# Kernel optimization log

Hardware: AMD Instinct MI355X
Metric: run time of the kernel (lower is better)

Reference implementation:

```python
import math
import jax, jax.numpy as jnp
import numpy as np

# static config (mirrors init_kwargs / input_specs)
B, HRV, WRV, CRV = 2, 32, 1024, 64
CB, HB, WB = 256, 200, 200
D, COUT, HEADS, POINTS = 128, 128, 8, 6
DH = D // HEADS
RMAX = 55.0
XMIN, XMAX, YMIN, YMAX = -50.0, 50.0, -50.0, 50.0


def group_norm(x, gamma, beta, groups, eps=1e-5):
    b, h, w, c = x.shape
    xg = x.reshape(b, h, w, groups, c // groups)
    mean = xg.mean(axis=(1, 2, 4), keepdims=True)
    var = xg.var(axis=(1, 2, 4), keepdims=True)
    xg = (xg - mean) * jax.lax.rsqrt(var + eps)
    return xg.reshape(b, h, w, c) * gamma + beta


def fwd(x_rv, bev, pq_w, pq_b, pv_w, pv_b, po_w, po_b, qs_w1, qs_b1, qs_w2, qs_b2,
        rh_w1, rh_b1, rh_g1, rh_be1, rh_w2, rh_g2, rh_be2, rh_w3, rh_b3,
        so_w, so_b, aw_w, aw_b, vp_w, vp_b, op_w, op_b):
    b = x_rv.shape[0]
    nq = HRV * WRV
    az = jnp.linspace(-math.pi, math.pi, WRV + 1)[:-1]  # [Wrv]
    az = jnp.broadcast_to(az[None, None, :], (b, HRV, WRV))
    coord = jnp.stack([jnp.sin(az), jnp.cos(az), jnp.zeros_like(az)], axis=-1)  # [b,H,W,3]
    Q0 = x_rv @ pq_w + pq_b                                  # 1x1 conv as matmul (NHWC)
    Vmap = bev.transpose(0, 2, 3, 1) @ pv_w + pv_b           # [b,HB,WB,D]
    # range head: 1x1 conv -> GN(8) -> GELU -> 3x3 circular conv -> GN(8) -> GELU -> 1x1 conv
    h = jnp.concatenate([x_rv, coord], axis=-1) @ rh_w1 + rh_b1
    h = jax.nn.gelu(group_norm(h, rh_g1, rh_be1, 8), approximate=False)
    hp = jnp.pad(h, ((0, 0), (1, 1), (1, 1), (0, 0)), mode='wrap')  # circular padding
    h = jax.lax.conv_general_dilated(hp, rh_w2, (1, 1), 'VALID',
                                     dimension_numbers=('NHWC', 'HWIO', 'NHWC'))
    h = jax.nn.gelu(group_norm(h, rh_g2, rh_be2, 8), approximate=False)
    rh = h @ rh_w3 + rh_b3                                   # [b,H,W,2]
    mu = jnp.clip(rh[..., 0], 0.0, RMAX)                     # [b,H,W]
    log_sigma = jnp.clip(rh[..., 1:2], -5.0, 3.0)            # [b,H,W,1]
    sigma = jnp.exp(log_sigma)
    x_mu = mu * jnp.cos(az)
    y_mu = mu * jnp.sin(az)
    rx = jnp.clip((x_mu - XMIN) / (XMAX - XMIN), 0.0, 1.0)
    ry = jnp.clip((y_mu - YMIN) / (YMAX - YMIN), 0.0, 1.0)
    ref = jnp.stack([rx, ry], axis=-1).reshape(b, nq, 2)
    sig_feat = jnp.concatenate([log_sigma, 1.0 / (sigma + 1e-6)], axis=-1)
    q = jnp.concatenate([Q0, sig_feat], axis=-1) @ qs_w1 + qs_b1
    q = jax.nn.gelu(q, approximate=False) @ qs_w2 + qs_b2
    query = q.reshape(b, nq, D)
    # ---- MSDA (num_levels = 1) ----
    value = Vmap.reshape(b, HB * WB, D) @ vp_w + vp_b
    vflat = value.reshape(b, HB * WB, HEADS, DH).transpose(0, 2, 1, 3)  # [b,heads,NV,dh]
    offs = (query @ so_w + so_b).reshape(b, nq, HEADS, POINTS, 2)
    attw = jax.nn.softmax((query @ aw_w + aw_b).reshape(b, nq, HEADS, POINTS), axis=-1)
    norm = jnp.array([WB, HB], dtype=query.dtype)            # offset_normalizer = [W, H]
    loc = ref[:, :, None, None, :] + offs / norm             # [b,nq,heads,P,2] in [0,1]
    loc = loc.transpose(0, 2, 1, 3, 4)                       # [b,heads,nq,P,2]
    attw = attw.transpose(0, 2, 1, 3)                        # [b,heads,nq,P]
    # grid_sample bilinear, zero padding, align_corners=False: pix = loc*size - 0.5
    px = loc[..., 0] * WB - 0.5
    py = loc[..., 1] * HB - 0.5
    x0 = jnp.floor(px).astype(jnp.int32)
    y0 = jnp.floor(py).astype(jnp.int32)
    wx = px - x0
    wy = py - y0

    def gather(xi, yi):
        valid = (xi >= 0) & (xi < WB) & (yi >= 0) & (yi < HB)
        idx = jnp.clip(yi, 0, HB - 1) * WB + jnp.clip(xi, 0, WB - 1)
        g = jnp.take_along_axis(vflat, idx.reshape(b, HEADS, nq * POINTS, 1), axis=2)
        return g.reshape(b, HEADS, nq, POINTS, DH) * valid[..., None]

    sampled = (gather(x0, y0) * ((1 - wx) * (1 - wy))[..., None]
               + gather(x0 + 1, y0) * (wx * (1 - wy))[..., None]
               + gather(x0, y0 + 1) * ((1 - wx) * wy)[..., None]
               + gather(x0 + 1, y0 + 1) * (wx * wy)[..., None])    # [b,heads,nq,P,dh]
    out = (sampled * attw[..., None]).sum(axis=3)                  # [b,heads,nq,dh]
    out = out.transpose(0, 2, 1, 3).reshape(b, nq, D) @ op_w + op_b
    y = out.reshape(b, HRV, WRV, D) @ po_w + po_b                  # proj_o (1x1 conv)
    return y                                                       # [b,Hrv,Wrv,C_out]


def setup_inputs() -> dict:
    key = jax.random.key(0)
    ks = jax.random.split(key, 20)
    def rn(i, shape, s=0.02):
        return s * jax.random.normal(ks[i], shape, jnp.float32)
    z = lambda n: jnp.zeros((n,), jnp.float32)
    o = lambda n: jnp.ones((n,), jnp.float32)
    return dict(
        x_rv=rn(0, (B, HRV, WRV, CRV), 1.0),
        bev=rn(1, (B, CB, HB, WB), 1.0),
        pq_w=rn(2, (CRV, D)), pq_b=z(D),
        pv_w=rn(3, (CB, D)), pv_b=z(D),
        po_w=rn(4, (D, COUT)), po_b=z(COUT),
        qs_w1=rn(5, (D + 2, D)), qs_b1=z(D),
        qs_w2=rn(6, (D, D)), qs_b2=z(D),
        rh_w1=rn(7, (CRV + 3, 128)), rh_b1=z(128),
        rh_g1=o(128), rh_be1=z(128),
        rh_w2=rn(8, (3, 3, 128, 64)),
        rh_g2=o(64), rh_be2=z(64),
        rh_w3=rn(9, (64, 2)), rh_b3=z(2),
        so_w=rn(10, (D, HEADS * POINTS * 2)), so_b=rn(11, (HEADS * POINTS * 2,), 0.5),
        aw_w=rn(12, (D, HEADS * POINTS)), aw_b=z(HEADS * POINTS),
        vp_w=rn(13, (D, D)), vp_b=z(D),
        op_w=rn(14, (D, D)), op_b=z(D),
    )


def reference(x_rv, bev, pq_w, pq_b, pv_w, pv_b, po_w, po_b, qs_w1, qs_b1, qs_w2, qs_b2,
              rh_w1, rh_b1, rh_g1, rh_be1, rh_w2, rh_g2, rh_be2, rh_w3, rh_b3,
              so_w, so_b, aw_w, aw_b, vp_w, vp_b, op_w, op_b):
    return fwd(x_rv, bev, pq_w, pq_b, pv_w, pv_b, po_w, po_b, qs_w1, qs_b1, qs_w2, qs_b2,
               rh_w1, rh_b1, rh_g1, rh_be1, rh_w2, rh_g2, rh_be2, rh_w3, rh_b3,
               so_w, so_b, aw_w, aw_b, vp_w, vp_b, op_w, op_b)
```

## Files before the change

### kernel.cpp

```cpp
#include <hip/hip_runtime.h>
#include <math.h>

#define PI_F 3.14159265358979323846f


typedef __attribute__((ext_vector_type(8))) short bf16x8;
typedef __attribute__((ext_vector_type(4))) float f32x4;

__device__ __forceinline__ float gelu_f(float x) {
    return 0.5f * x * (1.0f + erff(x * 0.70710678118654752440f));
}

__device__ __forceinline__ unsigned short f2bf(float x) {
    unsigned int u = __float_as_uint(x);
    u += 0x7fffu + ((u >> 16) & 1u);
    return (unsigned short)(u >> 16);
}

__device__ __forceinline__ float bf2f(unsigned short h) {
    return __uint_as_float((unsigned int)h << 16);
}

__global__ void prep_weights(const float* __restrict__ pv_w, const float* __restrict__ pv_b,
                             const float* __restrict__ vp_w, const float* __restrict__ vp_b,
                             const float* __restrict__ op_w, const float* __restrict__ op_b,
                             const float* __restrict__ po_w, const float* __restrict__ po_b,
                             const float* __restrict__ pq_w, const float* __restrict__ pq_b,
                             const float* __restrict__ qs_w1, const float* __restrict__ qs_b1,
                             const float* __restrict__ qs_w2, const float* __restrict__ qs_b2,
                             const float* __restrict__ so_w, const float* __restrict__ so_b,
                             const float* __restrict__ aw_w, const float* __restrict__ aw_b,
                             const float* __restrict__ rh_w2,
                             unsigned short* __restrict__ wvh, unsigned short* __restrict__ wvl,
                             float* __restrict__ pvvp_b,
                             float* __restrict__ oppo_w, float* __restrict__ oppo_b,
                             float* __restrict__ pqqs_w, float* __restrict__ pqqs_b,
                             float* __restrict__ qsso_w, float* __restrict__ qsso_b,
                             float* __restrict__ qsaw_w, float* __restrict__ qsaw_b,
                             unsigned short* __restrict__ wtb,
                             float2* __restrict__ azsc) {
    int r = blockIdx.x;
    int d = threadIdx.x;
    if (r < 256) {
        float s = 0.f;
        for (int k = 0; k < 128; ++k) s += pv_w[r * 128 + k] * vp_w[k * 128 + d];
        unsigned short h = f2bf(s);
        wvh[d * 256 + r] = h;
        wvl[d * 256 + r] = f2bf(s - bf2f(h));
    } else if (r == 256) {
        float s = vp_b[d];
        for (int k = 0; k < 128; ++k) s += pv_b[k] * vp_w[k * 128 + d];
        pvvp_b[d] = s;
    } else if (r < 385) {
        int rr = r - 257;
        float s = 0.f;
        for (int k = 0; k < 128; ++k) s += op_w[rr * 128 + k] * po_w[k * 128 + d];
        oppo_w[rr * 128 + d] = s;
    } else if (r == 385) {
        float s = po_b[d];
        for (int k = 0; k < 128; ++k) s += op_b[k] * po_w[k * 128 + d];
        oppo_b[d] = s;
    } else if (r < 450) {
        int rr = r - 386;
        float s = 0.f;
        for (int k = 0; k < 128; ++k) s += pq_w[rr * 128 + k] * qs_w1[k * 128 + d];
        pqqs_w[rr * 128 + d] = s;
    } else if (r == 450) {
        float s = qs_b1[d];
        for (int k = 0; k < 128; ++k) s += pq_b[k] * qs_w1[k * 128 + d];
        pqqs_b[d] = s;
    } else if (r < 459) {
        int w = (r - 451) * 128 + d;
        float az = -PI_F + (float)w * (6.283185307179586f / 1024.0f);
        azsc[w] = make_float2(sinf(az), cosf(az));
    } else if (r < 587) {
        int rr = r - 459;
        if (d < 96) {
            float s = 0.f;
            for (int k = 0; k < 128; ++k) s += qs_w2[rr * 128 + k] * so_w[k * 96 + d];
            qsso_w[rr * 96 + d] = s;
        }
    } else if (r == 587) {
        if (d < 96) {
            float s = so_b[d];
            for (int k = 0; k < 128; ++k) s += qs_b2[k] * so_w[k * 96 + d];
            qsso_b[d] = s;
        }
    } else if (r < 716) {
        int rr = r - 588;
        if (d < 48) {
            float s = 0.f;
            for (int k = 0; k < 128; ++k) s += qs_w2[rr * 128 + k] * aw_w[k * 48 + d];
            qsaw_w[rr * 48 + d] = s;
        }
    } else if (r == 716) {
        if (d < 48) {
            float s = aw_b[d];
            for (int k = 0; k < 128; ++k) s += qs_b2[k] * aw_w[k * 48 + d];
            qsaw_b[d] = s;
        }
    } else {
        int idx = (r - 717) * 128 + d;
        int ci = idx & 31;
        int o = (idx >> 5) & 63;
        int cc4i = (idx >> 11) & 3;
        int tap = idx >> 13;
        float w = rh_w2[((size_t)tap * 128 + cc4i * 32 + ci) * 64 + o];
        wtb[idx] = f2bf(w);
    }
}

template <int NT, bool STATS>
__global__ __launch_bounds__(2 * NT) void gemm_v3(
    const float* __restrict__ A, int lda,
    const float* __restrict__ W,
    const float* __restrict__ bias,
    float* __restrict__ C, int K,
    const float2* __restrict__ azsc,
    const float* __restrict__ extra2,
    const float* __restrict__ extra_w,
    int emode, int do_gelu, float* __restrict__ stats1) {
    constexpr int NTH = 2 * NT;
    constexpr int NTO = NT / 8;
    __shared__ float As[32][140];
    __shared__ float Ws[32][NT];
    __shared__ float sred[8][2];
    const int tid = threadIdx.x;
    const int tn = tid % NTO;
    const int tm = tid / NTO;
    const int m0 = blockIdx.x * 128;
    if (STATS && tid < 16) sred[tid >> 1][tid & 1] = 0.f;
    float acc[8][8];
#pragma unroll
    for (int i = 0; i < 8; ++i)
#pragma unroll
        for (int j = 0; j < 8; ++j) acc[i][j] = 0.f;

    for (int k0 = 0; k0 < K; k0 += 32) {
        __syncthreads();
        for (int f = tid; f < 1024; f += NTH) {
            int r = f >> 3, c4 = f & 7;
            float4 v = *(const float4*)(A + (size_t)(m0 + r) * lda + k0 + c4 * 4);
            As[c4 * 4 + 0][r] = v.x;
            As[c4 * 4 + 1][r] = v.y;
            As[c4 * 4 + 2][r] = v.z;
            As[c4 * 4 + 3][r] = v.w;
        }
        for (int f = tid; f < 8 * NT; f += NTH) {
            int kk = f / (NT / 4), n4 = f % (NT / 4);
            *(float4*)&Ws[kk][n4 * 4] = *(const float4*)(W + (size_t)(k0 + kk) * NT + n4 * 4);
        }
        __syncthreads();
#pragma unroll 2
        for (int k = 0; k < 32; ++k) {
            const float4 a0 = *(const float4*)&As[k][tm * 8];
            const float4 a1 = *(const float4*)&As[k][tm * 8 + 4];
            const float4 w0 = *(const float4*)&Ws[k][tn * 8];
            const float4 w1 = *(const float4*)&Ws[k][tn * 8 + 4];
            const float av[8] = {a0.x, a0.y, a0.z, a0.w, a1.x, a1.y, a1.z, a1.w};
            const float wv[8] = {w0.x, w0.y, w0.z, w0.w, w1.x, w1.y, w1.z, w1.w};
#pragma unroll
            for (int i = 0; i < 8; ++i)
#pragma unroll
                for (int j = 0; j < 8; ++j) acc[i][j] += av[i] * wv[j];
        }
    }
    float bv[8], e0w[8], e1w[8];
#pragma unroll
    for (int j = 0; j < 8; ++j) bv[j] = bias[tn * 8 + j];
    if (emode) {
#pragma unroll
        for (int j = 0; j < 8; ++j) {
            e0w[j] = extra_w[tn * 8 + j];
            e1w[j] = extra_w[NT + tn * 8 + j];
        }
    }
    float ts = 0.f, ts2 = 0.f;
#pragma unroll
    for (int i = 0; i < 8; ++i) {
        int m = m0 + tm * 8 + i;
        float e0 = 0.f, e1 = 0.f;
        if (emode == 1) {
            float2 sc = azsc[m & 1023];
            e0 = sc.x; e1 = sc.y;
        } else if (emode == 2) {
            e0 = extra2[2 * (size_t)m];
            e1 = extra2[2 * (size_t)m + 1];
        }
        float o[8];
#pragma unroll
        for (int j = 0; j < 8; ++j) {
            float v = acc[i][j] + bv[j];
            if (emode) v += e0 * e0w[j] + e1 * e1w[j];
            if (do_gelu) v = gelu_f(v);
            if (STATS) { ts += v; ts2 += v * v; }
            o[j] = v;
        }
        *(float4*)(C + (size_t)m * NT + tn * 8) = make_float4(o[0], o[1], o[2], o[3]);
        *(float4*)(C + (size_t)m * NT + tn * 8 + 4) = make_float4(o[4], o[5], o[6], o[7]);
    }
    if (STATS) {
        atomicAdd(&sred[tn >> 1][0], ts);
        atomicAdd(&sred[tn >> 1][1], ts2);
        __syncthreads();
        if (tid < 8) {
            int b = m0 >> 15;
            atomicAdd(&stats1[(b * 8 + tid) * 2 + 0], sred[tid][0]);
            atomicAdd(&stats1[(b * 8 + tid) * 2 + 1], sred[tid][1]);
        }
    }
}

template <int MT, int NT, int NTH>
__global__ __launch_bounds__(NTH) void gemm_rn(
    const float* __restrict__ A, int lda,
    const float* __restrict__ W, int ldw,
    const float* __restrict__ bias,
    float* __restrict__ C, int ldc, int K) {
    static_assert(NTH == (MT / 8) * (NT / 4), "thread count mismatch");
    __shared__ float As[32][MT + 12];
    __shared__ float Ws[32][NT];
    constexpr int NTN = NT / 4;
    const int tid = threadIdx.x;
    const int tn = tid % NTN;
    const int tm = tid / NTN;
    const int m0 = blockIdx.x * MT;
    float acc[8][4];
#pragma unroll
    for (int i = 0; i < 8; ++i)
#pragma unroll
        for (int j = 0; j < 4; ++j) acc[i][j] = 0.f;

    for (int k0 = 0; k0 < K; k0 += 32) {
        __syncthreads();
        for (int f = tid; f < MT * 8; f += NTH) {
            int r = f >> 3, c4 = f & 7;
            float4 v = *(const float4*)(A + (size_t)(m0 + r) * lda + k0 + c4 * 4);
            As[c4 * 4 + 0][r] = v.x;
            As[c4 * 4 + 1][r] = v.y;
            As[c4 * 4 + 2][r] = v.z;
            As[c4 * 4 + 3][r] = v.w;
        }
        for (int f = tid; f < 8 * NT; f += NTH) {
            int kk = f / NTN, n4 = f % NTN;
            *(float4*)&Ws[kk][n4 * 4] = *(const float4*)(W + (size_t)(k0 + kk) * ldw + n4 * 4);
        }
        __syncthreads();
#pragma unroll 4
        for (int k = 0; k < 32; ++k) {
            const float4 a0 = *(const float4*)&As[k][tm * 8];
            const float4 a1 = *(const float4*)&As[k][tm * 8 + 4];
            const float4 wv = *(const float4*)&Ws[k][tn * 4];
            acc[0][0] += a0.x * wv.x; acc[0][1] += a0.x * wv.y; acc[0][2] += a0.x * wv.z; acc[0][3] += a0.x * wv.w;
            acc[1][0] += a0.y * wv.x; acc[1][1] += a0.y * wv.y; acc[1][2] += a0.y * wv.z; acc[1][3] += a0.y * wv.w;
            acc[2][0] += a0.z * wv.x; acc[2][1] += a0.z * wv.y; acc[2][2] += a0.z * wv.z; acc[2][3] += a0.z * wv.w;
            acc[3][0] += a0.w * wv.x; acc[3][1] += a0.w * wv.y; acc[3][2] += a0.w * wv.z; acc[3][3] += a0.w * wv.w;
            acc[4][0] += a1.x * wv.x; acc[4][1] += a1.x * wv.y; acc[4][2] += a1.x * wv.z; acc[4][3] += a1.x * wv.w;
            acc[5][0] += a1.y * wv.x; acc[5][1] += a1.y * wv.y; acc[5][2] += a1.y * wv.z; acc[5][3] += a1.y * wv.w;
            acc[6][0] += a1.z * wv.x; acc[6][1] += a1.z * wv.y; acc[6][2] += a1.z * wv.z; acc[6][3] += a1.z * wv.w;
            acc[7][0] += a1.w * wv.x; acc[7][1] += a1.w * wv.y; acc[7][2] += a1.w * wv.z; acc[7][3] += a1.w * wv.w;
        }
    }
#pragma unroll
    for (int i = 0; i < 8; ++i) {
        int m = m0 + tm * 8 + i;
        float4 o;
        o.x = acc[i][0] + bias[tn * 4 + 0];
        o.y = acc[i][1] + bias[tn * 4 + 1];
        o.z = acc[i][2] + bias[tn * 4 + 2];
        o.w = acc[i][3] + bias[tn * 4 + 3];
        *(float4*)(C + (size_t)m * ldc + tn * 4) = o;
    }
}

__global__ __launch_bounds__(256) void value_gemm_mfma(
    const float* __restrict__ bev,
    const unsigned short* __restrict__ Wh, const unsigned short* __restrict__ Wl,
    const float* __restrict__ bf, float* __restrict__ V) {
    __shared__ __align__(16) short Ah_s[128 * 40];
    __shared__ __align__(16) short Al_s[128 * 40];
    __shared__ __align__(16) short Bh_s[128 * 40];
    __shared__ __align__(16) short Bl_s[128 * 40];
    const int tid = threadIdx.x;
    const int wid = tid >> 6;
    const int lane = tid & 63;
    const int m = lane & 15;
    const int quad = lane >> 4;
    const int n0 = blockIdx.x * 128;
    const int b = blockIdx.y;
    const float* bevb = bev + (size_t)b * 256 * 40000;
    const int wr = (wid >> 1) * 64;
    const int wc = (wid & 1) * 64;
    f32x4 acc[4][4];
#pragma unroll
    for (int i = 0; i < 4; ++i)
#pragma unroll
        for (int j = 0; j < 4; ++j) acc[i][j] = (f32x4){0.f, 0.f, 0.f, 0.f};

    const int sn = tid & 127;
    const int kq0 = (tid >> 7) * 2;
    int ng = n0 + sn;
    if (ng > 39999) ng = 39999;
    const float* srcA = bevb + ng;

    float va[2][8];
#define LOADA(K0)                                                        \
    {                                                                    \
        _Pragma("unroll")                                                \
        for (int i_ = 0; i_ < 2; ++i_) {                                 \
            const float* s_ = srcA + (size_t)((K0) + (kq0 + i_) * 8) * 40000; \
            _Pragma("unroll")                                            \
            for (int j_ = 0; j_ < 8; ++j_) va[i_][j_] = s_[(size_t)j_ * 40000]; \
        }                                                                \
    }

    LOADA(0);
    for (int k0 = 0; k0 < 256; k0 += 32) {
        __syncthreads();
#pragma unroll
        for (int i = 0; i < 2; ++i) {
            int k8 = kq0 + i;
            bf16x8 ph, pl;
#pragma unroll
            for (int j = 0; j < 8; ++j) {
                unsigned short h = f2bf(va[i][j]);
                ph[j] = (short)h;
                pl[j] = (short)f2bf(va[i][j] - bf2f(h));
            }
            *(bf16x8*)&Ah_s[sn * 40 + k8 * 8] = ph;
            *(bf16x8*)&Al_s[sn * 40 + k8 * 8] = pl;
        }
        if (k0 < 224) LOADA(k0 + 32);
        for (int f = tid; f < 512; f += 256) {
            int d = f >> 2, k8 = f & 3;
            uint4 vh = *(const uint4*)(Wh + (size_t)d * 256 + k0 + k8 * 8);
            uint4 vl = *(const uint4*)(Wl + (size_t)d * 256 + k0 + k8 * 8);
            *(uint4*)&Bh_s[d * 40 + k8 * 8] = vh;
            *(uint4*)&Bl_s[d * 40 + k8 * 8] = vl;
        }
        __syncthreads();
        bf16x8 ah[4], al[4], bh[4], bl[4];
#pragma unroll
        for (int r = 0; r < 4; ++r) {
            ah[r] = *(const bf16x8*)&Ah_s[(wr + r * 16 + m) * 40 + quad * 8];
            al[r] = *(const bf16x8*)&Al_s[(wr + r * 16 + m) * 40 + quad * 8];
            bh[r] = *(const bf16x8*)&Bh_s[(wc + r * 16 + m) * 40 + quad * 8];
            bl[r] = *(const bf16x8*)&Bl_s[(wc + r * 16 + m) * 40 + quad * 8];
        }
#pragma unroll
        for (int i = 0; i < 4; ++i)
#pragma unroll
            for (int j = 0; j < 4; ++j) {
                acc[i][j] = __builtin_amdgcn_mfma_f32_16x16x32_bf16(ah[i], bh[j], acc[i][j], 0, 0, 0);
                acc[i][j] = __builtin_amdgcn_mfma_f32_16x16x32_bf16(ah[i], bl[j], acc[i][j], 0, 0, 0);
                acc[i][j] = __builtin_amdgcn_mfma_f32_16x16x32_bf16(al[i], bh[j], acc[i][j], 0, 0, 0);
            }
    }
#undef LOADA
    float bv[4];
#pragma unroll
    for (int j = 0; j < 4; ++j) bv[j] = bf[wc + j * 16 + m];
#pragma unroll
    for (int i = 0; i < 4; ++i) {
        int nbase = n0 + wr + i * 16 + quad * 4;
#pragma unroll
        for (int r = 0; r < 4; ++r) {
            int n = nbase + r;
            if (n < 40000) {
                float* vp = V + ((size_t)b * 40000 + n) * 128 + wc + m;
#pragma unroll
                for (int j = 0; j < 4; ++j) vp[j * 16] = acc[i][j][r] + bv[j];
            }
        }
    }
}

__global__ __launch_bounds__(256) void gn1_bf16(
    const float* __restrict__ X, const float* __restrict__ stats,
    const float* __restrict__ g1, const float* __restrict__ be1,
    unsigned short* __restrict__ Ob) {
    size_t i4 = (size_t)blockIdx.x * 256 + threadIdx.x;
    size_t base = i4 * 4;
    int c = (int)(base & 127);
    int mrow = (int)(base >> 7);
    int b = mrow >> 15;
    int g = c >> 4;
    float mean = stats[(b * 8 + g) * 2 + 0] * (1.0f / 524288.0f);
    float var = stats[(b * 8 + g) * 2 + 1] * (1.0f / 524288.0f) - mean * mean;
    float rs = 1.0f / sqrtf(var + 1e-5f);
    float4 x = *(const float4*)(X + base);
    float4 gm = *(const float4*)(g1 + c);
    float4 bt = *(const float4*)(be1 + c);
    ushort4 o;
    o.x = f2bf(gelu_f((x.x - mean) * rs * gm.x + bt.x));
    o.y = f2bf(gelu_f((x.y - mean) * rs * gm.y + bt.y));
    o.z = f2bf(gelu_f((x.z - mean) * rs * gm.z + bt.z));
    o.w = f2bf(gelu_f((x.w - mean) * rs * gm.w + bt.w));
    *(ushort4*)(Ob + base) = o;
}

__global__ __launch_bounds__(256, 4) void conv3x3_mfma(
    const unsigned short* __restrict__ H1b,
    const unsigned short* __restrict__ Wtb,
    float* __restrict__ Y,
    float* __restrict__ stats2) {
    __shared__ short As_s[66 * 40];
    __shared__ short Ws_s[3 * 64 * 40];
    __shared__ float sred[8][2];
    const int tid = threadIdx.x;
    const int wid = tid >> 6;
    const int lane = tid & 63;
    const int m = lane & 15;
    const int quad = lane >> 4;
    const int x0 = blockIdx.x * 64;
    const int y = blockIdx.y;
    const int b = blockIdx.z;
    if (tid < 16) sred[tid >> 1][tid & 1] = 0.f;
    f32x4 acc[4];
#pragma unroll
    for (int oq = 0; oq < 4; ++oq) acc[oq] = (f32x4){0.f, 0.f, 0.f, 0.f};

    const unsigned short* Hb = H1b + (size_t)b * 32 * 1024 * 128;
    for (int ry = 0; ry < 3; ++ry) {
        const int gy = (y + ry + 31) & 31;
        const unsigned short* Hrow = Hb + (size_t)gy * 1024 * 128;
        for (int cc4 = 0; cc4 < 4; ++cc4) {
            __syncthreads();
            for (int f = tid; f < 264; f += 256) {
                int xx = f >> 2, cq = f & 3;
                int gx = (x0 + xx + 1023) & 1023;
                uint4 v = *(const uint4*)(Hrow + (size_t)gx * 128 + cc4 * 32 + cq * 8);
                *(uint4*)&As_s[xx * 40 + cq * 8] = v;
            }
            for (int f = tid; f < 768; f += 256) {
                int cq = f & 3, o = (f >> 2) & 63, dx = f >> 8;
                int tap = ry * 3 + dx;
                uint4 v = *(const uint4*)(Wtb + ((size_t)(tap * 4 + cc4) * 64 + o) * 32 + cq * 8);
                *(uint4*)&Ws_s[(dx * 64 + o) * 40 + cq * 8] = v;
            }
            __syncthreads();
            const int arow = wid * 16 + m;
#pragma unroll
            for (int dx = 0; dx < 3; ++dx) {
                bf16x8 a = *(const bf16x8*)&As_s[(arow + dx) * 40 + quad * 8];
#pragma unroll
                for (int oq = 0; oq < 4; ++oq) {
                    bf16x8 bfr = *(const bf16x8*)&Ws_s[(dx * 64 + oq * 16 + m) * 40 + quad * 8];
                    acc[oq] = __builtin_amdgcn_mfma_f32_16x16x32_bf16(a, bfr, acc[oq], 0, 0, 0);
                }
            }
        }
    }
    float sv[4], qv[4];
#pragma unroll
    for (int oq = 0; oq < 4; ++oq) {
        sv[oq] = acc[oq].x + acc[oq].y + acc[oq].z + acc[oq].w;
        qv[oq] = acc[oq].x * acc[oq].x + acc[oq].y * acc[oq].y +
                 acc[oq].z * acc[oq].z + acc[oq].w * acc[oq].w;
    }
    const int masks[5] = {1, 2, 4, 16, 32};
#pragma unroll
    for (int mi = 0; mi < 5; ++mi) {
#pragma unroll
        for (int oq = 0; oq < 4; ++oq) {
            sv[oq] += __shfl_xor(sv[oq], masks[mi]);
            qv[oq] += __shfl_xor(qv[oq], masks[mi]);
        }
    }
    if ((lane & 55) == 0) {
        int gb = (lane >> 3) & 1;
#pragma unroll
        for (int oq = 0; oq < 4; ++oq) {
            atomicAdd(&sred[oq * 2 + gb][0], sv[oq]);
            atomicAdd(&sred[oq * 2 + gb][1], qv[oq]);
        }
    }
    const int pxb = x0 + wid * 16 + quad * 4;
    float* Yb = Y + ((size_t)(b * 32 + y) * 1024 + pxb) * 64;
#pragma unroll
    for (int oq = 0; oq < 4; ++oq) {
        const float av[4] = {acc[oq].x, acc[oq].y, acc[oq].z, acc[oq].w};
#pragma unroll
        for (int r = 0; r < 4; ++r) Yb[(size_t)r * 64 + oq * 16 + m] = av[r];
    }
    __syncthreads();
    if (tid < 16)
        atomicAdd(&stats2[(b * 8 + (tid >> 1)) * 2 + (tid & 1)], sred[tid >> 1][tid & 1]);
}

__global__ __launch_bounds__(256) void rh3_kernel(
    const float* __restrict__ H2, const float* __restrict__ stats,
    const float* __restrict__ gamma, const float* __restrict__ beta, float inv_cnt,
    const float* __restrict__ w3, const float* __restrict__ b3,
    const float2* __restrict__ azsc,
    float2* __restrict__ refxy, float2* __restrict__ sigf) {
    const int tid = threadIdx.x;
    const int lane = tid & 15;
    const int m = blockIdx.x * 16 + (tid >> 4);
    const int b = m >> 15;
    const int c = lane * 4;
    const int g = c >> 3;
    float mean = stats[(b * 8 + g) * 2 + 0] * inv_cnt;
    float var = stats[(b * 8 + g) * 2 + 1] * inv_cnt - mean * mean;
    float rs = 1.0f / sqrtf(var + 1e-5f);
    float4 v = *(const float4*)(H2 + (size_t)m * 64 + c);
    float hv[4];
    hv[0] = gelu_f((v.x - mean) * rs * gamma[c + 0] + beta[c + 0]);
    hv[1] = gelu_f((v.y - mean) * rs * gamma[c + 1] + beta[c + 1]);
    hv[2] = gelu_f((v.z - mean) * rs * gamma[c + 2] + beta[c + 2]);
    hv[3] = gelu_f((v.w - mean) * rs * gamma[c + 3] + beta[c + 3]);
    float d0 = 0.f, d1 = 0.f;
#pragma unroll
    for (int k = 0; k < 4; ++k) {
        d0 += hv[k] * w3[(c + k) * 2 + 0];
        d1 += hv[k] * w3[(c + k) * 2 + 1];
    }
#pragma unroll
    for (int s = 1; s < 16; s <<= 1) {
        d0 += __shfl_xor(d0, s, 16);
        d1 += __shfl_xor(d1, s, 16);
    }
    if (lane == 0) {
        float mu = fminf(fmaxf(d0 + b3[0], 0.f), 55.f);
        float ls = fminf(fmaxf(d1 + b3[1], -5.f), 3.f);
        float sg = expf(ls);
        float2 sc = azsc[m & 1023];
        float rx = fminf(fmaxf(mu * sc.y * 0.01f + 0.5f, 0.f), 1.f);
        float ry = fminf(fmaxf(mu * sc.x * 0.01f + 0.5f, 0.f), 1.f);
        refxy[m] = make_float2(rx, ry);
        sigf[m] = make_float2(ls, 1.f / (sg + 1e-6f));
    }
}

__global__ __launch_bounds__(256) void msda_kernel(
    const float* __restrict__ V, const float2* __restrict__ refxy,
    const float* __restrict__ offs, const float* __restrict__ aw,
    float* __restrict__ out) {
    const int tid = threadIdx.x;
    const int l4 = tid & 3;
    const int grp = tid >> 2;
    const int m = blockIdx.x * 8 + (grp >> 3);
    const int head = grp & 7;
    const int b = m >> 15;
    float2 r = refxy[m];
    const float* lg = aw + (size_t)m * 48 + head * 6;
    float l[6];
#pragma unroll
    for (int p = 0; p < 6; ++p) l[p] = lg[p];
    float mx = l[0];
#pragma unroll
    for (int p = 1; p < 6; ++p) mx = fmaxf(mx, l[p]);
    float s = 0.f;
#pragma unroll
    for (int p = 0; p < 6; ++p) { l[p] = expf(l[p] - mx); s += l[p]; }
    float inv = 1.f / s;
#pragma unroll
    for (int p = 0; p < 6; ++p) l[p] *= inv;
    const float* of = offs + (size_t)m * 96 + head * 12;
    const float* Vb = V + (size_t)b * 40000 * 128 + head * 16 + l4 * 4;
    const float bx = r.x * 200.f - 0.5f;
    const float by = r.y * 200.f - 0.5f;
    f32x4 acc = (f32x4){0.f, 0.f, 0.f, 0.f};
#pragma unroll
    for (int p = 0; p < 6; ++p) {
        float px = bx + of[p * 2 + 0];
        float py = by + of[p * 2 + 1];
        float fx = floorf(px), fy = floorf(py);
        int x0 = (int)fx, y0 = (int)fy;
        float wx = px - fx, wy = py - fy;
        int xc0 = min(max(x0, 0), 199), xc1 = min(max(x0 + 1, 0), 199);
        int yc0 = min(max(y0, 0), 199), yc1 = min(max(y0 + 1, 0), 199);
        bool vx0 = ((unsigned)x0 < 200u), vx1 = ((unsigned)(x0 + 1) < 200u);
        bool vy0 = ((unsigned)y0 < 200u), vy1 = ((unsigned)(y0 + 1) < 200u);
        const f32x4 v00 = *(const f32x4*)(Vb + ((size_t)(yc0 * 200 + xc0)) * 128);
        const f32x4 v10 = *(const f32x4*)(Vb + ((size_t)(yc0 * 200 + xc1)) * 128);
        const f32x4 v01 = *(const f32x4*)(Vb + ((size_t)(yc1 * 200 + xc0)) * 128);
        const f32x4 v11 = *(const f32x4*)(Vb + ((size_t)(yc1 * 200 + xc1)) * 128);
        float w = l[p];
        float w00 = (vx0 && vy0) ? w * (1.f - wx) * (1.f - wy) : 0.f;
        float w10 = (vx1 && vy0) ? w * wx * (1.f - wy) : 0.f;
        float w01 = (vx0 && vy1) ? w * (1.f - wx) * wy : 0.f;
        float w11 = (vx1 && vy1) ? w * wx * wy : 0.f;
        acc += v00 * w00;
        acc += v10 * w10;
        acc += v01 * w01;
        acc += v11 * w11;
    }
    *(f32x4*)(out + (size_t)m * 128 + head * 16 + l4 * 4) = acc;
}

extern "C" void kernel_launch(void* const* d_in, const int* in_sizes, int n_in,
                              void* d_out, int out_size, void* d_ws, size_t ws_size,
                              hipStream_t stream) {
    const float* x_rv = (const float*)d_in[0];
    const float* bev = (const float*)d_in[1];
    const float* pq_w = (const float*)d_in[2];
    const float* pq_b = (const float*)d_in[3];
    const float* pv_w = (const float*)d_in[4];
    const float* pv_b = (const float*)d_in[5];
    const float* po_w = (const float*)d_in[6];
    const float* po_b = (const float*)d_in[7];
    const float* qs_w1 = (const float*)d_in[8];
    const float* qs_b1 = (const float*)d_in[9];
    const float* qs_w2 = (const float*)d_in[10];
    const float* qs_b2 = (const float*)d_in[11];
    const float* rh_w1 = (const float*)d_in[12];
    const float* rh_b1 = (const float*)d_in[13];
    const float* rh_g1 = (const float*)d_in[14];
    const float* rh_be1 = (const float*)d_in[15];
    const float* rh_w2 = (const float*)d_in[16];
    const float* rh_g2 = (const float*)d_in[17];
    const float* rh_be2 = (const float*)d_in[18];
    const float* rh_w3 = (const float*)d_in[19];
    const float* rh_b3 = (const float*)d_in[20];
    const float* so_w = (const float*)d_in[21];
    const float* so_b = (const float*)d_in[22];
    const float* aw_w = (const float*)d_in[23];
    const float* aw_b = (const float*)d_in[24];
    const float* vp_w = (const float*)d_in[25];
    const float* vp_b = (const float*)d_in[26];
    const float* op_w = (const float*)d_in[27];
    const float* op_b = (const float*)d_in[28];

    const int M = 65536;

    float* ws = (float*)d_ws;
    float* azsc = ws;    ws += 2048;
    unsigned short* wvh = (unsigned short*)ws; ws += 16384;
    unsigned short* wvl = (unsigned short*)ws; ws += 16384;
    float* pvvp_b = ws;  ws += 128;
    float* oppo_w = ws;  ws += 128 * 128;
    float* oppo_b = ws;  ws += 128;
    float* pqqs_w = ws;  ws += 64 * 128;
    float* pqqs_b = ws;  ws += 128;
    float* qsso_w = ws;  ws += 128 * 96;
    float* qsso_b = ws;  ws += 128;
    float* qsaw_w = ws;  ws += 128 * 48;
    float* qsaw_b = ws;  ws += 64;
    float* stats = ws;   ws += 64;
    unsigned short* wtb = (unsigned short*)ws;  ws += 36864;
    unsigned short* h1b = (unsigned short*)ws;  ws += (size_t)M * 64;
    float* Vv = ws;      ws += (size_t)80000 * 128;
    float* h1 = ws;      ws += (size_t)M * 128;
    float* h2 = ws;      ws += (size_t)M * 64;
    float* q1 = ws;      ws += (size_t)M * 128;
    float* refxy = ws;   ws += (size_t)M * 2;
    float* sigf = ws;    ws += (size_t)M * 2;
    size_t need_bytes = (size_t)(ws - (float*)d_ws) * sizeof(float);
    if (ws_size < need_bytes) return;
    float* offs = h1;
    float* attw = h2;
    float* mo = q1;

    float2* azsc2 = (float2*)azsc;
    float2* refxy2 = (float2*)refxy;
    float2* sigf2 = (float2*)sigf;

    prep_weights<<<1293, 128, 0, stream>>>(
        pv_w, pv_b, vp_w, vp_b, op_w, op_b, po_w, po_b, pq_w, pq_b,
        qs_w1, qs_b1, qs_w2, qs_b2, so_w, so_b, aw_w, aw_b, rh_w2,
        wvh, wvl, pvvp_b, oppo_w, oppo_b, pqqs_w, pqqs_b,
        qsso_w, qsso_b, qsaw_w, qsaw_b, wtb, azsc2);
    hipMemsetAsync(stats, 0, 64 * sizeof(float), stream);

    gemm_v3<128, true><<<M / 128, 256, 0, stream>>>(
        x_rv, 64, rh_w1, rh_b1, h1, 64, azsc2, nullptr, rh_w1 + 64 * 128, 1, 0, stats);

    value_gemm_mfma<<<dim3(313, 2), 256, 0, stream>>>(bev, wvh, wvl, pvvp_b, Vv);

    gn1_bf16<<<8192, 256, 0, stream>>>(h1, stats, rh_g1, rh_be1, h1b);

    conv3x3_mfma<<<dim3(16, 32, 2), 256, 0, stream>>>(h1b, wtb, h2, stats + 32);

    rh3_kernel<<<4096, 256, 0, stream>>>(h2, stats + 32, rh_g2, rh_be2, 1.0f / 262144.0f,
                                         rh_w3, rh_b3, azsc2, refxy2, sigf2);

    gemm_v3<128, false><<<M / 128, 256, 0, stream>>>(
        x_rv, 64, pqqs_w, pqqs_b, q1, 64, nullptr, sigf, qs_w1 + 128 * 128, 2, 1, nullptr);

    gemm_v3<96, false><<<M / 128, 192, 0, stream>>>(
        q1, 128, qsso_w, qsso_b, offs, 128, nullptr, nullptr, nullptr, 0, 0, nullptr);

    gemm_rn<128, 48, 192><<<M / 128, 192, 0, stream>>>(
        q1, 128, qsaw_w, 48, qsaw_b, attw, 48, 128);

    msda_kernel<<<M / 8, 256, 0, stream>>>(Vv, refxy2, offs, attw, mo);

    gemm_v3<128, false><<<M / 128, 256, 0, stream>>>(
        mo, 128, oppo_w, oppo_b, (float*)d_out, 128, nullptr, nullptr, nullptr, 0, 0, nullptr);
}
```

Measured before the change: 480.1 us.

## Restructure BEV value GEMM: 64-row tiles, register-resident weights, double-buffered LDS

Cuts the value-projection tile from 128 to 64 rows, which doubles the grid to 625x2 blocks. Each wave now loads its bf16 hi/lo weight fragments straight from global memory into registers instead of staging them in LDS. The A tile is double-buffered in LDS so each k-step needs one barrier instead of two. The hi/lo bf16 split is now done with bit masking and a packed convert instruction rather than per-element rounding, and the bounds check is dropped because 40000 divides evenly by 64. In exchange, weight reads hit global or cache more often and each wave reuses less data per k-step.

```diff
diff --git a/kernel.cpp b/kernel.cpp
--- a/kernel.cpp
+++ b/kernel.cpp
@@ -277,100 +277,115 @@
     const float* __restrict__ bev,
     const unsigned short* __restrict__ Wh, const unsigned short* __restrict__ Wl,
     const float* __restrict__ bf, float* __restrict__ V) {
-    __shared__ __align__(16) short Ah_s[128 * 40];
-    __shared__ __align__(16) short Al_s[128 * 40];
-    __shared__ __align__(16) short Bh_s[128 * 40];
-    __shared__ __align__(16) short Bl_s[128 * 40];
+    __shared__ __align__(16) short Ah0_s[64 * 40];
+    __shared__ __align__(16) short Al0_s[64 * 40];
+    __shared__ __align__(16) short Ah1_s[64 * 40];
+    __shared__ __align__(16) short Al1_s[64 * 40];
     const int tid = threadIdx.x;
     const int wid = tid >> 6;
     const int lane = tid & 63;
     const int m = lane & 15;
     const int quad = lane >> 4;
-    const int n0 = blockIdx.x * 128;
+    const int n0 = blockIdx.x * 64;
     const int b = blockIdx.y;
-    const float* bevb = bev + (size_t)b * 256 * 40000;
-    const int wr = (wid >> 1) * 64;
+    const int wr = (wid >> 1) * 32;
     const int wc = (wid & 1) * 64;
-    f32x4 acc[4][4];
-#pragma unroll
-    for (int i = 0; i < 4; ++i)
+    f32x4 acc[2][4];
+#pragma unroll
+    for (int i = 0; i < 2; ++i)
 #pragma unroll
         for (int j = 0; j < 4; ++j) acc[i][j] = (f32x4){0.f, 0.f, 0.f, 0.f};
 
-    const int sn = tid & 127;
-    const int kq0 = (tid >> 7) * 2;
-    int ng = n0 + sn;
-    if (ng > 39999) ng = 39999;
-    const float* srcA = bevb + ng;
-
-    float va[2][8];
-#define LOADA(K0)                                                        \
-    {                                                                    \
-        _Pragma("unroll")                                                \
-        for (int i_ = 0; i_ < 2; ++i_) {                                 \
-            const float* s_ = srcA + (size_t)((K0) + (kq0 + i_) * 8) * 40000; \
-            _Pragma("unroll")                                            \
-            for (int j_ = 0; j_ < 8; ++j_) va[i_][j_] = s_[(size_t)j_ * 40000]; \
-        }                                                                \
-    }
-
-    LOADA(0);
-    for (int k0 = 0; k0 < 256; k0 += 32) {
-        __syncthreads();
+    const int sn = tid & 63;
+    const int kq = tid >> 6;
+    const float* srcA = bev + (size_t)b * 256 * 40000 + n0 + sn;
+    const unsigned short* pBh[4];
+    const unsigned short* pBl[4];
+#pragma unroll
+    for (int j = 0; j < 4; ++j) {
+        size_t off = (size_t)(wc + j * 16 + m) * 256 + quad * 8;
+        pBh[j] = Wh + off;
+        pBl[j] = Wl + off;
+    }
+
+    float va[8];
+    bf16x8 vbh[4], vbl[4];
+#pragma unroll
+    for (int j = 0; j < 8; ++j) va[j] = srcA[(size_t)(kq * 8 + j) * 40000];
+#pragma unroll
+    for (int j = 0; j < 4; ++j) {
+        vbh[j] = *(const bf16x8*)(pBh[j]);
+        vbl[j] = *(const bf16x8*)(pBl[j]);
+    }
+
+    short* pAh = Ah0_s; short* pAl = Al0_s;
+    short* qAh = Ah1_s; short* qAl = Al1_s;
+
+    for (int t = 0; t < 8; ++t) {
+        const int k0 = t * 32;
+        uint4 ph, pl;
+        {
+            unsigned hp[4], lp[4];
+#pragma unroll
+            for (int pj = 0; pj < 4; ++pj) {
+                float x0 = va[2 * pj], x1 = va[2 * pj + 1];
+                unsigned u0 = __float_as_uint(x0), u1 = __float_as_uint(x1);
+                hp[pj] = __builtin_amdgcn_perm(u1, u0, 0x07060302);
+                float h0 = __uint_as_float(u0 & 0xffff0000u);
+                float h1 = __uint_as_float(u1 & 0xffff0000u);
+                float l0 = x0 - h0, l1 = x1 - h1;
+                asm("v_cvt_pk_bf16_f32 %0, %1, %2" : "=v"(lp[pj]) : "v"(l0), "v"(l1));
+            }
+            ph = make_uint4(hp[0], hp[1], hp[2], hp[3]);
+            pl = make_uint4(lp[0], lp[1], lp[2], lp[3]);
+        }
+        *(uint4*)&pAh[sn * 40 + kq * 8] = ph;
+        *(uint4*)&pAl[sn * 40 + kq * 8] = pl;
+        if (t < 7) {
+#pragma unroll
+            for (int j = 0; j < 8; ++j)
+                va[j] = srcA[(size_t)(k0 + 32 + kq * 8 + j) * 40000];
+        }
+        asm volatile("s_waitcnt lgkmcnt(0)" ::: "memory");
+        __builtin_amdgcn_sched_barrier(0);
+        __builtin_amdgcn_s_barrier();
+        __builtin_amdgcn_sched_barrier(0);
+        bf16x8 ah[2], al[2];
 #pragma unroll
         for (int i = 0; i < 2; ++i) {
-            int k8 = kq0 + i;
-            bf16x8 ph, pl;
-#pragma unroll
-            for (int j = 0; j < 8; ++j) {
-                unsigned short h = f2bf(va[i][j]);
-                ph[j] = (short)h;
-                pl[j] = (short)f2bf(va[i][j] - bf2f(h));
+            ah[i] = *(const bf16x8*)&pAh[(wr + i * 16 + m) * 40 + quad * 8];
+            al[i] = *(const bf16x8*)&pAl[(wr + i * 16 + m) * 40 + quad * 8];
+        }
+#pragma unroll
+        for (int i = 0; i < 2; ++i)
+#pragma unroll
+            for (int j = 0; j < 4; ++j) {
+                acc[i][j] = __builtin_amdgcn_mfma_f32_16x16x32_bf16(ah[i], vbh[j], acc[i][j], 0, 0, 0);
+                acc[i][j] = __builtin_amdgcn_mfma_f32_16x16x32_bf16(ah[i], vbl[j], acc[i][j], 0, 0, 0);
+                acc[i][j] = __builtin_amdgcn_mfma_f32_16x16x32_bf16(al[i], vbh[j], acc[i][j], 0, 0, 0);
             }
-            *(bf16x8*)&Ah_s[sn * 40 + k8 * 8] = ph;
-            *(bf16x8*)&Al_s[sn * 40 + k8 * 8] = pl;
-        }
-        if (k0 < 224) LOADA(k0 + 32);
-        for (int f = tid; f < 512; f += 256) {
-            int d = f >> 2, k8 = f & 3;
-            uint4 vh = *(const uint4*)(Wh + (size_t)d * 256 + k0 + k8 * 8);
-            uint4 vl = *(const uint4*)(Wl + (size_t)d * 256 + k0 + k8 * 8);
-            *(uint4*)&Bh_s[d * 40 + k8 * 8] = vh;
-            *(uint4*)&Bl_s[d * 40 + k8 * 8] = vl;
-        }
-        __syncthreads();
-        bf16x8 ah[4], al[4], bh[4], bl[4];
-#pragma unroll
-        for (int r = 0; r < 4; ++r) {
-            ah[r] = *(const bf16x8*)&Ah_s[(wr + r * 16 + m) * 40 + quad * 8];
-            al[r] = *(const bf16x8*)&Al_s[(wr + r * 16 + m) * 40 + quad * 8];
-            bh[r] = *(const bf16x8*)&Bh_s[(wc + r * 16 + m) * 40 + quad * 8];
-            bl[r] = *(const bf16x8*)&Bl_s[(wc + r * 16 + m) * 40 + quad * 8];
-        }
-#pragma unroll
-        for (int i = 0; i < 4; ++i)
+        if (t < 7) {
 #pragma unroll
             for (int j = 0; j < 4; ++j) {
-                acc[i][j] = __builtin_amdgcn_mfma_f32_16x16x32_bf16(ah[i], bh[j], acc[i][j], 0, 0, 0);
-                acc[i][j] = __builtin_amdgcn_mfma_f32_16x16x32_bf16(ah[i], bl[j], acc[i][j], 0, 0, 0);
-                acc[i][j] = __builtin_amdgcn_mfma_f32_16x16x32_bf16(al[i], bh[j], acc[i][j], 0, 0, 0);
+                vbh[j] = *(const bf16x8*)(pBh[j] + k0 + 32);
+                vbl[j] = *(const bf16x8*)(pBl[j] + k0 + 32);
             }
-    }
-#undef LOADA
+        }
+        short* th = pAh; pAh = qAh; qAh = th;
+        short* tl = pAl; pAl = qAl; qAl = tl;
+    }
     float bv[4];
 #pragma unroll
     for (int j = 0; j < 4; ++j) bv[j] = bf[wc + j * 16 + m];
 #pragma unroll
-    for (int i = 0; i < 4; ++i) {
+    for (int i = 0; i < 2; ++i) {
         int nbase = n0 + wr + i * 16 + quad * 4;
 #pragma unroll
         for (int r = 0; r < 4; ++r) {
             int n = nbase + r;
-            if (n < 40000) {
-                float* vp = V + ((size_t)b * 40000 + n) * 128 + wc + m;
-#pragma unroll
-                for (int j = 0; j < 4; ++j) vp[j * 16] = acc[i][j][r] + bv[j];
-            }
+            float* vp = V + ((size_t)b * 40000 + n) * 128 + wc + m;
+#pragma unroll
+            for (int j = 0; j < 4; ++j) vp[j * 16] = acc[i][j][r] + bv[j];
         }
     }
 }
@@ -666,7 +681,7 @@
     gemm_v3<128, true><<<M / 128, 256, 0, stream>>>(
         x_rv, 64, rh_w1, rh_b1, h1, 64, azsc2, nullptr, rh_w1 + 64 * 128, 1, 0, stats);
 
-    value_gemm_mfma<<<dim3(313, 2), 256, 0, stream>>>(bev, wvh, wvl, pvvp_b, Vv);
+    value_gemm_mfma<<<dim3(625, 2), 256, 0, stream>>>(bev, wvh, wvl, pvvp_b, Vv);
 
     gn1_bf16<<<8192, 256, 0, stream>>>(h1, stats, rh_g1, rh_be1, h1b);
 
```

Result: no change. 486.2 us (+1.3%).

## Pre-transpose BEV into bf16 hi/lo NK layout and stream value GEMM from global

Applied to the files above, without the earlier changes.

Adds a separate kernel that transposes the channel-major BEV tensor through shared memory into row-major bf16 high/low split arrays. The value-projection GEMM then reads A and B fragments straight from global memory with register double-buffering instead of staging them in LDS, using smaller 64-row tiles. This targets the strided, uncoalesced column reads and the in-loop conversion of the old kernel. In exchange it adds an extra pass that writes and rereads the BEV data and reuses the h1 scratch buffer, so the value GEMM is moved ahead of the range-head GEMM.

```diff
diff --git a/kernel.cpp b/kernel.cpp
--- a/kernel.cpp
+++ b/kernel.cpp
@@ -110,6 +110,51 @@
     }
 }
 
+__global__ __launch_bounds__(256) void bev_transpose(
+    const float* __restrict__ bev,
+    unsigned short* __restrict__ bvh, unsigned short* __restrict__ bvl) {
+    __shared__ float T[32 * 257];
+    const int t = threadIdx.x;
+    const int wave = t >> 6, lane = t & 63;
+    const int n0 = blockIdx.x * 256;
+    const int k0 = blockIdx.y * 32;
+    const int b = blockIdx.z;
+    const float* src = bev + (size_t)b * 256 * 40000;
+#pragma unroll
+    for (int i = 0; i < 8; ++i) {
+        int kk = i * 4 + wave;
+        int nl = n0 + lane * 4;
+        if (nl > 39996) nl = 39996;
+        float4 v = *(const float4*)(src + (size_t)(k0 + kk) * 40000 + nl);
+        *(float4*)&T[kk * 257 + lane * 4] = v;
+    }
+    __syncthreads();
+    const int kp = t & 3;
+    const int nr0 = t >> 2;
+#pragma unroll
+    for (int p = 0; p < 4; ++p) {
+        int nrow = p * 64 + nr0;
+        int n = n0 + nrow;
+        float f[8];
+#pragma unroll
+        for (int j = 0; j < 8; ++j) f[j] = T[(kp * 8 + j) * 257 + nrow];
+        unsigned hh[4], ll[4];
+#pragma unroll
+        for (int q = 0; q < 4; ++q) {
+            unsigned u0 = __float_as_uint(f[2 * q]), u1 = __float_as_uint(f[2 * q + 1]);
+            hh[q] = __builtin_amdgcn_perm(u1, u0, 0x07060302);
+            float l0 = f[2 * q] - __uint_as_float(u0 & 0xffff0000u);
+            float l1 = f[2 * q + 1] - __uint_as_float(u1 & 0xffff0000u);
+            asm("v_cvt_pk_bf16_f32 %0, %1, %2" : "=v"(ll[q]) : "v"(l0), "v"(l1));
+        }
+        if (n < 40000) {
+            size_t o = ((size_t)b * 40000 + n) * 256 + k0 + kp * 8;
+            *(uint4*)(bvh + o) = make_uint4(hh[0], hh[1], hh[2], hh[3]);
+            *(uint4*)(bvl + o) = make_uint4(ll[0], ll[1], ll[2], ll[3]);
+        }
+    }
+}
+
 template <int NT, bool STATS>
 __global__ __launch_bounds__(2 * NT) void gemm_v3(
     const float* __restrict__ A, int lda,
@@ -274,103 +319,83 @@
 }
 
 __global__ __launch_bounds__(256) void value_gemm_mfma(
-    const float* __restrict__ bev,
+    const unsigned short* __restrict__ Ah, const unsigned short* __restrict__ Al,
     const unsigned short* __restrict__ Wh, const unsigned short* __restrict__ Wl,
     const float* __restrict__ bf, float* __restrict__ V) {
-    __shared__ __align__(16) short Ah_s[128 * 40];
-    __shared__ __align__(16) short Al_s[128 * 40];
-    __shared__ __align__(16) short Bh_s[128 * 40];
-    __shared__ __align__(16) short Bl_s[128 * 40];
     const int tid = threadIdx.x;
     const int wid = tid >> 6;
     const int lane = tid & 63;
     const int m = lane & 15;
     const int quad = lane >> 4;
-    const int n0 = blockIdx.x * 128;
+    const int n0 = blockIdx.x * 64;
     const int b = blockIdx.y;
-    const float* bevb = bev + (size_t)b * 256 * 40000;
-    const int wr = (wid >> 1) * 64;
+    const int wr = (wid >> 1) * 32;
     const int wc = (wid & 1) * 64;
-    f32x4 acc[4][4];
-#pragma unroll
-    for (int i = 0; i < 4; ++i)
+    f32x4 acc[2][4];
+#pragma unroll
+    for (int i = 0; i < 2; ++i)
 #pragma unroll
         for (int j = 0; j < 4; ++j) acc[i][j] = (f32x4){0.f, 0.f, 0.f, 0.f};
 
-    const int sn = tid & 127;
-    const int kq0 = (tid >> 7) * 2;
-    int ng = n0 + sn;
-    if (ng > 39999) ng = 39999;
-    const float* srcA = bevb + ng;
-
-    float va[2][8];
-#define LOADA(K0)                                                        \
-    {                                                                    \
-        _Pragma("unroll")                                                \
-        for (int i_ = 0; i_ < 2; ++i_) {                                 \
-            const float* s_ = srcA + (size_t)((K0) + (kq0 + i_) * 8) * 40000; \
-            _Pragma("unroll")                                            \
-            for (int j_ = 0; j_ < 8; ++j_) va[i_][j_] = s_[(size_t)j_ * 40000]; \
-        }                                                                \
-    }
-
-    LOADA(0);
-    for (int k0 = 0; k0 < 256; k0 += 32) {
-        __syncthreads();
-#pragma unroll
-        for (int i = 0; i < 2; ++i) {
-            int k8 = kq0 + i;
-            bf16x8 ph, pl;
-#pragma unroll
-            for (int j = 0; j < 8; ++j) {
-                unsigned short h = f2bf(va[i][j]);
-                ph[j] = (short)h;
-                pl[j] = (short)f2bf(va[i][j] - bf2f(h));
-            }
-            *(bf16x8*)&Ah_s[sn * 40 + k8 * 8] = ph;
-            *(bf16x8*)&Al_s[sn * 40 + k8 * 8] = pl;
-        }
-        if (k0 < 224) LOADA(k0 + 32);
-        for (int f = tid; f < 512; f += 256) {
-            int d = f >> 2, k8 = f & 3;
-            uint4 vh = *(const uint4*)(Wh + (size_t)d * 256 + k0 + k8 * 8);
-            uint4 vl = *(const uint4*)(Wl + (size_t)d * 256 + k0 + k8 * 8);
-            *(uint4*)&Bh_s[d * 40 + k8 * 8] = vh;
-            *(uint4*)&Bl_s[d * 40 + k8 * 8] = vl;
-        }
-        __syncthreads();
-        bf16x8 ah[4], al[4], bh[4], bl[4];
-#pragma unroll
-        for (int r = 0; r < 4; ++r) {
-            ah[r] = *(const bf16x8*)&Ah_s[(wr + r * 16 + m) * 40 + quad * 8];
-            al[r] = *(const bf16x8*)&Al_s[(wr + r * 16 + m) * 40 + quad * 8];
-            bh[r] = *(const bf16x8*)&Bh_s[(wc + r * 16 + m) * 40 + quad * 8];
-            bl[r] = *(const bf16x8*)&Bl_s[(wc + r * 16 + m) * 40 + quad * 8];
-        }
-#pragma unroll
-        for (int i = 0; i < 4; ++i)
-#pragma unroll
-            for (int j = 0; j < 4; ++j) {
-                acc[i][j] = __builtin_amdgcn_mfma_f32_16x16x32_bf16(ah[i], bh[j], acc[i][j], 0, 0, 0);
-                acc[i][j] = __builtin_amdgcn_mfma_f32_16x16x32_bf16(ah[i], bl[j], acc[i][j], 0, 0, 0);
-                acc[i][j] = __builtin_amdgcn_mfma_f32_16x16x32_bf16(al[i], bh[j], acc[i][j], 0, 0, 0);
-            }
-    }
-#undef LOADA
+    size_t aoff[2], boff[4];
+#pragma unroll
+    for (int i = 0; i < 2; ++i)
+        aoff[i] = ((size_t)b * 40000 + n0 + wr + i * 16 + m) * 256 + quad * 8;
+#pragma unroll
+    for (int j = 0; j < 4; ++j)
+        boff[j] = (size_t)(wc + j * 16 + m) * 256 + quad * 8;
+
+    bf16x8 a0h[2], a0l[2], b0h[4], b0l[4];
+    bf16x8 a1h[2], a1l[2], b1h[4], b1l[4];
+
+#define LOADSET(AH, AL, BH, BL, K0)                              \
+    {                                                            \
+        _Pragma("unroll")                                        \
+        for (int i_ = 0; i_ < 2; ++i_) {                         \
+            AH[i_] = *(const bf16x8*)(Ah + aoff[i_] + (K0));     \
+            AL[i_] = *(const bf16x8*)(Al + aoff[i_] + (K0));     \
+        }                                                        \
+        _Pragma("unroll")                                        \
+        for (int j_ = 0; j_ < 4; ++j_) {                         \
+            BH[j_] = *(const bf16x8*)(Wh + boff[j_] + (K0));     \
+            BL[j_] = *(const bf16x8*)(Wl + boff[j_] + (K0));     \
+        }                                                        \
+    }
+#define MFMASET(AH, AL, BH, BL)                                                              \
+    {                                                                                        \
+        _Pragma("unroll")                                                                    \
+        for (int i_ = 0; i_ < 2; ++i_)                                                       \
+        _Pragma("unroll")                                                                    \
+        for (int j_ = 0; j_ < 4; ++j_) {                                                     \
+            acc[i_][j_] = __builtin_amdgcn_mfma_f32_16x16x32_bf16(AH[i_], BH[j_], acc[i_][j_], 0, 0, 0); \
+            acc[i_][j_] = __builtin_amdgcn_mfma_f32_16x16x32_bf16(AH[i_], BL[j_], acc[i_][j_], 0, 0, 0); \
+            acc[i_][j_] = __builtin_amdgcn_mfma_f32_16x16x32_bf16(AL[i_], BH[j_], acc[i_][j_], 0, 0, 0); \
+        }                                                                                    \
+    }
+
+    LOADSET(a0h, a0l, b0h, b0l, 0);
+    LOADSET(a1h, a1l, b1h, b1l, 32);
+#pragma unroll
+    for (int tt = 0; tt < 4; ++tt) {
+        MFMASET(a0h, a0l, b0h, b0l);
+        if (tt < 3) LOADSET(a0h, a0l, b0h, b0l, tt * 64 + 64);
+        MFMASET(a1h, a1l, b1h, b1l);
+        if (tt < 3) LOADSET(a1h, a1l, b1h, b1l, tt * 64 + 96);
+    }
+#undef LOADSET
+#undef MFMASET
     float bv[4];
 #pragma unroll
     for (int j = 0; j < 4; ++j) bv[j] = bf[wc + j * 16 + m];
 #pragma unroll
-    for (int i = 0; i < 4; ++i) {
+    for (int i = 0; i < 2; ++i) {
         int nbase = n0 + wr + i * 16 + quad * 4;
 #pragma unroll
         for (int r = 0; r < 4; ++r) {
             int n = nbase + r;
-            if (n < 40000) {
-                float* vp = V + ((size_t)b * 40000 + n) * 128 + wc + m;
-#pragma unroll
-                for (int j = 0; j < 4; ++j) vp[j * 16] = acc[i][j][r] + bv[j];
-            }
+            float* vp = V + ((size_t)b * 40000 + n) * 128 + wc + m;
+#pragma unroll
+            for (int j = 0; j < 4; ++j) vp[j * 16] = acc[i][j][r] + bv[j];
         }
     }
 }
@@ -651,6 +676,8 @@
     float* offs = h1;
     float* attw = h2;
     float* mo = q1;
+    unsigned short* bvh = (unsigned short*)h1;
+    unsigned short* bvl = (unsigned short*)(h1 + 10240000);
 
     float2* azsc2 = (float2*)azsc;
     float2* refxy2 = (float2*)refxy;
@@ -663,11 +690,13 @@
         qsso_w, qsso_b, qsaw_w, qsaw_b, wtb, azsc2);
     hipMemsetAsync(stats, 0, 64 * sizeof(float), stream);
 
+    bev_transpose<<<dim3(157, 8, 2), 256, 0, stream>>>(bev, bvh, bvl);
+
+    value_gemm_mfma<<<dim3(625, 2), 256, 0, stream>>>(bvh, bvl, wvh, wvl, pvvp_b, Vv);
+
     gemm_v3<128, true><<<M / 128, 256, 0, stream>>>(
         x_rv, 64, rh_w1, rh_b1, h1, 64, azsc2, nullptr, rh_w1 + 64 * 128, 1, 0, stats);
 
-    value_gemm_mfma<<<dim3(313, 2), 256, 0, stream>>>(bev, wvh, wvl, pvvp_b, Vv);
-
     gn1_bf16<<<8192, 256, 0, stream>>>(h1, stats, rh_g1, rh_be1, h1b);
 
     conv3x3_mfma<<<dim3(16, 32, 2), 256, 0, stream>>>(h1b, wtb, h2, stats + 32);
```

Result: slower. 524.3 us (+9.2%).
